# Performance work log

Hardware: AMD Instinct MI355X
Metric: run time of the kernel (lower is better)

The kernel has to match this reference:

```python
import jax, jax.numpy as jnp
import numpy as np

B, S, D = 2, 2048, 1024
H = 16
HD = D // H  # 64


def setup_inputs() -> dict:
    key = jax.random.key(0)
    ks = jax.random.split(key, 9)
    s = 1.0 / np.sqrt(D)
    return {
        "query_input": jax.random.normal(ks[0], (B, S, D), dtype=jnp.float32),
        "Wq": jax.random.normal(ks[1], (D, D), dtype=jnp.float32) * s,
        "bq": jax.random.normal(ks[2], (D,), dtype=jnp.float32) * 0.02,
        "Wk": jax.random.normal(ks[3], (D, D), dtype=jnp.float32) * s,
        "bk": jax.random.normal(ks[4], (D,), dtype=jnp.float32) * 0.02,
        "Wv": jax.random.normal(ks[5], (D, D), dtype=jnp.float32) * s,
        "bv": jax.random.normal(ks[6], (D,), dtype=jnp.float32) * 0.02,
        "Wo": jax.random.normal(ks[7], (D, D), dtype=jnp.float32) * s,
        "bo": jax.random.normal(ks[8], (D,), dtype=jnp.float32) * 0.02,
    }


def _split_heads(x):
    # [B, S, D] -> [B, H, S, HD]
    return x.reshape(B, S, H, HD).transpose(0, 2, 1, 3)


def reference(query_input, Wq, bq, Wk, bk, Wv, bv, Wo, bo):
    # self-attention: key_value_input = query_input
    q = _split_heads(query_input @ Wq + bq)
    k = _split_heads(query_input @ Wk + bk)
    v = _split_heads(query_input @ Wv + bv)
    scores = jnp.einsum("bhqd,bhkd->bhqk", q, k) / jnp.sqrt(jnp.float32(HD))
    probs = jax.nn.softmax(scores, axis=-1)  # dropout is identity in eval
    ctx = jnp.einsum("bhqk,bhkd->bhqd", probs, v)
    ctx = ctx.transpose(0, 2, 1, 3).reshape(B, S, D)
    return ctx @ Wo + bo
```

## Files before the change

### kernel.cpp

```cpp
#include <hip/hip_runtime.h>
#include <hip/hip_bf16.h>
#include <cstdint>

constexpr int Bsz = 2, Seq = 2048, Dim = 1024, NH = 16, HDim = 64;
constexpr int Mtok = Bsz * Seq;
constexpr int NQKV = 3 * Dim;
constexpr float QSCALE = 0.125f * 1.4426950408889634f;

typedef __attribute__((ext_vector_type(4))) float f32x4;
typedef __attribute__((ext_vector_type(16))) float f32x16;
typedef __attribute__((ext_vector_type(8))) short bf16x8;

#if __has_builtin(__builtin_amdgcn_exp2f)
#define EXP2(x) __builtin_amdgcn_exp2f(x)
#else
#define EXP2(x) exp2f(x)
#endif

__device__ __forceinline__ ushort f2bf(float f) {
    union { float f; uint32_t u; } v; v.f = f;
    uint32_t u = v.u;
    uint32_t r = (u + 0x7fffu + ((u >> 16) & 1u)) >> 16;
    return (ushort)r;
}

__device__ __forceinline__ uint cvt_pk_bf16(float lo, float hi) {
    uint r;
    asm("v_cvt_pk_bf16_f32 %0, %1, %2" : "=v"(r) : "v"(lo), "v"(hi));
    return r;
}

__device__ __forceinline__ void gll16(const ushort* g, ushort* l) {
    __builtin_amdgcn_global_load_lds(
        (const __attribute__((address_space(1))) void*)g,
        (__attribute__((address_space(3))) void*)l, 16, 0, 0);
}

__global__ void convert_x(const float* __restrict__ in, ushort* __restrict__ out, int n16) {
    int i = blockIdx.x * 256 + threadIdx.x;
    if (i >= n16) return;
    int e = i * 16;
    int row = e >> 10;
    int k = e & 1023;
    int k0 = k & ~31;
    int c = (k >> 3) & 3;
    int sw = row & 3;
    const float4* p = (const float4*)(in + e);
    float4 a = p[0], b = p[1], c2 = p[2], d = p[3];
    uint4 o0, o1;
    o0.x = (uint)f2bf(a.x) | ((uint)f2bf(a.y) << 16);
    o0.y = (uint)f2bf(a.z) | ((uint)f2bf(a.w) << 16);
    o0.z = (uint)f2bf(b.x) | ((uint)f2bf(b.y) << 16);
    o0.w = (uint)f2bf(b.z) | ((uint)f2bf(b.w) << 16);
    o1.x = (uint)f2bf(c2.x) | ((uint)f2bf(c2.y) << 16);
    o1.y = (uint)f2bf(c2.z) | ((uint)f2bf(c2.w) << 16);
    o1.z = (uint)f2bf(d.x) | ((uint)f2bf(d.y) << 16);
    o1.w = (uint)f2bf(d.z) | ((uint)f2bf(d.w) << 16);
    ushort* dstrow = out + (size_t)row * 1024 + k0;
    *(uint4*)(dstrow + ((c ^ sw) << 3))       = o0;
    *(uint4*)(dstrow + (((c + 1) ^ sw) << 3)) = o1;
}

__global__ void transpose_w4(const float* __restrict__ Wq, const float* __restrict__ Wk,
                             const float* __restrict__ Wv, const float* __restrict__ Wo,
                             ushort* __restrict__ Wtqkv, ushort* __restrict__ Wto) {
    __shared__ float tile[32][33];
    int z = blockIdx.z;
    const float* src = (z == 0) ? Wq : (z == 1) ? Wk : (z == 2) ? Wv : Wo;
    ushort* dst = (z == 3) ? Wto : Wtqkv + (size_t)z * 1024 * 1024;
    float scale = (z == 0) ? QSCALE : 1.f;
    int bx = blockIdx.x * 32, by = blockIdx.y * 32;
    int tx = threadIdx.x, ty = threadIdx.y;
#pragma unroll
    for (int j = 0; j < 32; j += 8)
        tile[ty + j][tx] = src[(size_t)(by + ty + j) * Dim + bx + tx];
    __syncthreads();
    int c = tx >> 3, wn8 = tx & 7;
#pragma unroll
    for (int j = 0; j < 32; j += 8) {
        int n = bx + ty + j;
        dst[(size_t)n * Dim + by + ((c ^ (n & 3)) << 3) + wn8] = f2bf(tile[tx][ty + j] * scale);
    }
}

__global__ void concat_bias(const float* __restrict__ bq, const float* __restrict__ bk,
                            const float* __restrict__ bv, float* __restrict__ dst) {
    int i = blockIdx.x * 256 + threadIdx.x;
    if (i >= NQKV) return;
    float v = (i < 1024) ? bq[i] * QSCALE : (i < 2048 ? bk[i - 1024] : bv[i - 2048]);
    dst[i] = v;
}

template <bool F32OUT>
__global__ __launch_bounds__(256) void gemm_bt(const ushort* __restrict__ A,
                                               const ushort* __restrict__ Bt,
                                               const float* __restrict__ bias,
                                               void* __restrict__ Cout,
                                               int Msz, int Nsz, int Ksz) {
    __shared__ ushort As[2][128 * 32];
    __shared__ ushort Bs[2][128 * 32];
    const int tid = threadIdx.x;
    const int lane = tid & 63, wid = tid >> 6;
    const int wm = wid >> 1, wn = wid & 1;
    const int bm = blockIdx.x * 128, bn = blockIdx.y * 128;
    const int g = lane >> 4, r16 = lane & 15;

    f32x4 acc[4][4] = {};

    const int srow = tid >> 2;
    const int sc = tid & 3;
    const ushort* ga0 = A + (size_t)(bm + srow) * Ksz + sc * 8;
    const ushort* ga1 = A + (size_t)(bm + 64 + srow) * Ksz + sc * 8;
    const ushort* gb0 = Bt + (size_t)(bn + srow) * Ksz + sc * 8;
    const ushort* gb1 = Bt + (size_t)(bn + 64 + srow) * Ksz + sc * 8;
    const int lofs = wid << 9;

#define GSTAGE(bufi, k_)  do {                          \
        gll16(ga0 + (k_), &As[bufi][lofs]);             \
        gll16(ga1 + (k_), &As[bufi][2048 + lofs]);      \
        gll16(gb0 + (k_), &Bs[bufi][lofs]);             \
        gll16(gb1 + (k_), &Bs[bufi][2048 + lofs]);      \
    } while (0)

    GSTAGE(0, 0);
    int cur = 0;

    for (int k0 = 0; k0 < Ksz; k0 += 32) {
        __syncthreads();
        if (k0 + 32 < Ksz) GSTAGE(cur ^ 1, k0 + 32);
        const ushort* Asb = As[cur];
        const ushort* Bsb = Bs[cur];
        bf16x8 af[4], bfr[4];
#pragma unroll
        for (int mt = 0; mt < 4; mt++) {
            int row = wm * 64 + mt * 16 + r16;
            af[mt] = *(const bf16x8*)(Asb + row * 32 + ((g ^ (row & 3)) * 8));
        }
#pragma unroll
        for (int nt = 0; nt < 4; nt++) {
            int row = wn * 64 + nt * 16 + r16;
            bfr[nt] = *(const bf16x8*)(Bsb + row * 32 + ((g ^ (row & 3)) * 8));
        }
#pragma unroll
        for (int mt = 0; mt < 4; mt++)
#pragma unroll
            for (int nt = 0; nt < 4; nt++)
                acc[mt][nt] = __builtin_amdgcn_mfma_f32_16x16x32_bf16(af[mt], bfr[nt], acc[mt][nt], 0, 0, 0);
        cur ^= 1;
    }
#undef GSTAGE

#pragma unroll
    for (int nt = 0; nt < 4; nt++) {
        int col = bn + wn * 64 + nt * 16 + r16;
        float bv = bias[col];
#pragma unroll
        for (int mt = 0; mt < 4; mt++) {
            int row0 = bm + wm * 64 + mt * 16 + g * 4;
            f32x4 c = acc[mt][nt];
#pragma unroll
            for (int i = 0; i < 4; i++) {
                float v = c[i] + bv;
                if (F32OUT)
                    ((float*)Cout)[(size_t)(row0 + i) * Nsz + col] = v;
                else
                    ((ushort*)Cout)[(size_t)(row0 + i) * Nsz + col] = f2bf(v);
            }
        }
    }
}

__global__ __launch_bounds__(256) void pack_kv(const ushort* __restrict__ QKV,
                                               ushort* __restrict__ Kp,
                                               ushort* __restrict__ Vp) {
    __shared__ ushort t[64][72];
    int bh = blockIdx.y, b = bh >> 4, h = bh & 15;
    int s0 = blockIdx.x * 64;
    int tid = threadIdx.x;
    int r = tid >> 2, c = tid & 3;
    const ushort* ksrc = QKV + (size_t)(b * Seq + s0 + r) * NQKV + 1024 + h * 64;
    ushort* kdst = Kp + ((size_t)bh * Seq + s0 + r) * 64;
    int sw = r & 7;
    *(uint4*)(kdst + ((c ^ sw) * 8))       = *(const uint4*)(ksrc + c * 8);
    *(uint4*)(kdst + (((c + 4) ^ sw) * 8)) = *(const uint4*)(ksrc + (c + 4) * 8);
    const ushort* vsrc = QKV + (size_t)(b * Seq + s0 + r) * NQKV + 2048 + h * 64;
    *(uint4*)(&t[r][c * 16])     = *(const uint4*)(vsrc + c * 16);
    *(uint4*)(&t[r][c * 16 + 8]) = *(const uint4*)(vsrc + c * 16 + 8);
    __syncthreads();
    int d = tid >> 2, cq = tid & 3;
    uint u[8];
#pragma unroll
    for (int jj = 0; jj < 8; jj++)
        u[jj] = (uint)t[cq * 16 + jj * 2][d] | ((uint)t[cq * 16 + jj * 2 + 1][d] << 16);
    int swd = d & 7;
    ushort* vdst = Vp + ((size_t)bh * Seq + s0) * 64 + d * 64;
    *(uint4*)(vdst + (((cq * 2) ^ swd) * 8))     = make_uint4(u[0], u[1], u[2], u[3]);
    *(uint4*)(vdst + (((cq * 2 + 1) ^ swd) * 8)) = make_uint4(u[4], u[5], u[6], u[7]);
}

__global__ __launch_bounds__(256) void attn(const ushort* __restrict__ QKV,
                                            const ushort* __restrict__ Kp,
                                            const ushort* __restrict__ Vp,
                                            ushort* __restrict__ Ctx) {
    __shared__ ushort Ks[2][64 * 64];
    __shared__ ushort Vs[2][64 * 64];
    __shared__ float Rl[4][32];
    const int tid = threadIdx.x, lane = tid & 63, w = tid >> 6;
    const int bh = blockIdx.y, b = bh >> 4, h = bh & 15;
    const int l31 = lane & 31, hi = lane >> 5, sw7 = l31 & 7;
    const bool lo = (hi == 0);
    const int qrow = blockIdx.x * 128 + w * 32;

    const ushort* Qr = QKV + (size_t)(b * Seq + qrow + l31) * NQKV + h * 64;
    bf16x8 qf[4];
#pragma unroll
    for (int ks = 0; ks < 4; ks++)
        qf[ks] = *(const bf16x8*)(Qr + ks * 16 + hi * 8);

    const ushort* KpB = Kp + (size_t)bh * Seq * 64;
    const ushort* VpB = Vp + (size_t)bh * Seq * 64;
    const int wb = w * 512;

#define STAGE(bufi, kv0_)  do {                                        \
        const ushort* ks_ = KpB + (size_t)(kv0_) * 64 + tid * 8;       \
        const ushort* vs_ = VpB + (size_t)(kv0_) * 64 + tid * 8;       \
        gll16(ks_,        &Ks[bufi][wb]);                              \
        gll16(ks_ + 2048, &Ks[bufi][2048 + wb]);                       \
        gll16(vs_,        &Vs[bufi][wb]);                              \
        gll16(vs_ + 2048, &Vs[bufi][2048 + wb]);                       \
    } while (0)

    STAGE(0, 0);

    f32x16 c0 = {}, c1 = {};
    float l_run = 0.f;
    int cur = 0;

    for (int kv0 = 0; kv0 < Seq; kv0 += 64) {
        __syncthreads();
        if (kv0 + 64 < Seq) STAGE(cur ^ 1, kv0 + 64);
        const ushort* Kt = Ks[cur];
        const ushort* Vt = Vs[cur];

        f32x16 s0, s1;
#pragma unroll
        for (int r = 0; r < 16; r++) { s0[r] = -8.f; s1[r] = -8.f; }
        __builtin_amdgcn_s_setprio(1);
#pragma unroll
        for (int ks = 0; ks < 4; ks++) {
            int ch = ((ks * 2 + hi) ^ sw7) << 3;
            bf16x8 k0 = *(const bf16x8*)(Kt + l31 * 64 + ch);
            bf16x8 k1 = *(const bf16x8*)(Kt + (32 + l31) * 64 + ch);
            s0 = __builtin_amdgcn_mfma_f32_32x32x16_bf16(k0, qf[ks], s0, 0, 0, 0);
            s1 = __builtin_amdgcn_mfma_f32_32x32x16_bf16(k1, qf[ks], s1, 0, 0, 0);
        }
        __builtin_amdgcn_s_setprio(0);

        float p0[16], p1[16];
        float ls0 = 0.f, ls1 = 0.f;
#pragma unroll
        for (int r = 0; r < 16; r++) {
            p0[r] = EXP2(s0[r]);
            p1[r] = EXP2(s1[r]);
            ls0 += p0[r]; ls1 += p1[r];
        }
        l_run += ls0 + ls1;

        bf16x8 pa[4];
#pragma unroll
        for (int sl = 0; sl < 4; sl++) {
            const float* pp = (sl < 2) ? p0 : p1;
            int rb = (sl & 1) * 8;
            uint x  = cvt_pk_bf16(pp[rb + 0], pp[rb + 1]);
            uint x2 = cvt_pk_bf16(pp[rb + 2], pp[rb + 3]);
            uint y  = cvt_pk_bf16(pp[rb + 4], pp[rb + 5]);
            uint y2 = cvt_pk_bf16(pp[rb + 6], pp[rb + 7]);
            uint v1 = lo ? y : x;
            uint v2 = lo ? y2 : x2;
            uint sv1 = (uint)__shfl_xor((int)v1, 32);
            uint sv2 = (uint)__shfl_xor((int)v2, 32);
            union { uint u[4]; bf16x8 v; } fr;
            fr.u[0] = lo ? x  : sv1;
            fr.u[1] = lo ? x2 : sv2;
            fr.u[2] = lo ? sv1 : y;
            fr.u[3] = lo ? sv2 : y2;
            pa[sl] = fr.v;
        }

        __builtin_amdgcn_s_setprio(1);
#pragma unroll
        for (int sl = 0; sl < 4; sl++) {
            int ch = ((sl * 2 + hi) ^ sw7) << 3;
            bf16x8 vf0 = *(const bf16x8*)(Vt + l31 * 64 + ch);
            bf16x8 vf1 = *(const bf16x8*)(Vt + (32 + l31) * 64 + ch);
            c0 = __builtin_amdgcn_mfma_f32_32x32x16_bf16(pa[sl], vf0, c0, 0, 0, 0);
            c1 = __builtin_amdgcn_mfma_f32_32x32x16_bf16(pa[sl], vf1, c1, 0, 0, 0);
        }
        __builtin_amdgcn_s_setprio(0);
        cur ^= 1;
    }
#undef STAGE

    float lt = l_run + __shfl_xor(l_run, 32);
    if (lo) Rl[w][l31] = 1.f / lt;
    __builtin_amdgcn_s_waitcnt(0);
    float rlv[16];
#pragma unroll
    for (int r = 0; r < 16; r++)
        rlv[r] = Rl[w][(r & 3) + 8 * (r >> 2) + 4 * hi];

    const int rowbase = b * Seq + qrow;
    const int cl = l31 >> 3, c7 = l31 & 7;
#pragma unroll
    for (int r = 0; r < 16; r++) {
        int q = (r & 3) + 8 * (r >> 2) + 4 * hi;
        int row = rowbase + q;
        int col0 = h * 64 + ((cl ^ (row & 3)) << 3) + c7;
        int col1 = h * 64 + 32 + ((cl ^ (row & 3)) << 3) + c7;
        Ctx[(size_t)row * Dim + col0] = f2bf(c0[r] * rlv[r]);
        Ctx[(size_t)row * Dim + col1] = f2bf(c1[r] * rlv[r]);
    }
}

extern "C" void kernel_launch(void* const* d_in, const int* in_sizes, int n_in,
                              void* d_out, int out_size, void* d_ws, size_t ws_size,
                              hipStream_t stream) {
    const float* X  = (const float*)d_in[0];
    const float* Wq = (const float*)d_in[1];
    const float* bq = (const float*)d_in[2];
    const float* Wk = (const float*)d_in[3];
    const float* bk = (const float*)d_in[4];
    const float* Wv = (const float*)d_in[5];
    const float* bv = (const float*)d_in[6];
    const float* Wo = (const float*)d_in[7];
    const float* bo = (const float*)d_in[8];

    char* ws = (char*)d_ws;
    ushort* Xb    = (ushort*)(ws);
    ushort* Wtqkv = (ushort*)(ws + 8388608);
    ushort* Wto   = (ushort*)(ws + 14680064);
    float*  bqkv  = (float*)(ws + 16777216);
    ushort* QKVb  = (ushort*)(ws + 16793600);
    ushort* Vp    = (ushort*)(ws + 41959424);
    ushort* Ctxb  = (ushort*)(ws + 50348032);
    ushort* Kp    = Xb;

    convert_x<<<1024, 256, 0, stream>>>(X, Xb, Mtok * Dim / 16);
    transpose_w4<<<dim3(32, 32, 4), dim3(32, 8), 0, stream>>>(Wq, Wk, Wv, Wo, Wtqkv, Wto);
    concat_bias<<<12, 256, 0, stream>>>(bq, bk, bv, bqkv);

    gemm_bt<false><<<dim3(32, 24), 256, 0, stream>>>(Xb, Wtqkv, bqkv, QKVb, Mtok, NQKV, Dim);
    pack_kv<<<dim3(32, 32), 256, 0, stream>>>(QKVb, Kp, Vp);
    attn<<<dim3(16, 32), 256, 0, stream>>>(QKVb, Kp, Vp, Ctxb);
    gemm_bt<true><<<dim3(32, 8), 256, 0, stream>>>(Ctxb, Wto, bo, (float*)d_out, Mtok, Dim, Dim);
}
```

Measured before the change: 135.9 us.

## Split attention KV range in two and add a combine kernel

Attention is split along the key/value sequence into two halves via blockIdx.z, doubling the block count from 512 to 1024 so the 256 CUs get more work and better occupancy. Each half writes unnormalized fp32 partial context and row sums. A new combine kernel adds the halves, normalizes, and writes the swizzled bf16 context. This works because the kernel uses a fixed max offset rather than a running max. The cost is extra fp32 traffic (about 32 MB written and read) and one more kernel launch.

Result: slower. 146.1 us (+7.5%).

```diff
diff --git a/kernel.cpp b/kernel.cpp
--- a/kernel.cpp
+++ b/kernel.cpp
@@ -201,15 +201,18 @@
 __global__ __launch_bounds__(256) void attn(const ushort* __restrict__ QKV,
                                             const ushort* __restrict__ Kp,
                                             const ushort* __restrict__ Vp,
-                                            ushort* __restrict__ Ctx) {
+                                            float* __restrict__ P0,
+                                            float* __restrict__ P1,
+                                            float* __restrict__ Lb) {
     __shared__ ushort Ks[2][64 * 64];
     __shared__ ushort Vs[2][64 * 64];
-    __shared__ float Rl[4][32];
     const int tid = threadIdx.x, lane = tid & 63, w = tid >> 6;
     const int bh = blockIdx.y, b = bh >> 4, h = bh & 15;
+    const int z = blockIdx.z;
     const int l31 = lane & 31, hi = lane >> 5, sw7 = l31 & 7;
     const bool lo = (hi == 0);
     const int qrow = blockIdx.x * 128 + w * 32;
+    const int kvbeg = z << 10, kvend = kvbeg + 1024;
 
     const ushort* Qr = QKV + (size_t)(b * Seq + qrow + l31) * NQKV + h * 64;
     bf16x8 qf[4];
@@ -230,15 +233,15 @@
         gll16(vs_ + 2048, &Vs[bufi][2048 + wb]);                       \
     } while (0)
 
-    STAGE(0, 0);
+    STAGE(0, kvbeg);
 
     f32x16 c0 = {}, c1 = {};
     float l_run = 0.f;
     int cur = 0;
 
-    for (int kv0 = 0; kv0 < Seq; kv0 += 64) {
+    for (int kv0 = kvbeg; kv0 < kvend; kv0 += 64) {
         __syncthreads();
-        if (kv0 + 64 < Seq) STAGE(cur ^ 1, kv0 + 64);
+        if (kv0 + 64 < kvend) STAGE(cur ^ 1, kv0 + 64);
         const ushort* Kt = Ks[cur];
         const ushort* Vt = Vs[cur];
 
@@ -302,24 +305,37 @@
 #undef STAGE
 
     float lt = l_run + __shfl_xor(l_run, 32);
-    if (lo) Rl[w][l31] = 1.f / lt;
-    __builtin_amdgcn_s_waitcnt(0);
-    float rlv[16];
-#pragma unroll
-    for (int r = 0; r < 16; r++)
-        rlv[r] = Rl[w][(r & 3) + 8 * (r >> 2) + 4 * hi];
-
     const int rowbase = b * Seq + qrow;
-    const int cl = l31 >> 3, c7 = l31 & 7;
+    if (lo) Lb[((size_t)z * Mtok + rowbase + l31) * NH + h] = lt;
+    float* Pout = z ? P1 : P0;
 #pragma unroll
     for (int r = 0; r < 16; r++) {
         int q = (r & 3) + 8 * (r >> 2) + 4 * hi;
-        int row = rowbase + q;
-        int col0 = h * 64 + ((cl ^ (row & 3)) << 3) + c7;
-        int col1 = h * 64 + 32 + ((cl ^ (row & 3)) << 3) + c7;
-        Ctx[(size_t)row * Dim + col0] = f2bf(c0[r] * rlv[r]);
-        Ctx[(size_t)row * Dim + col1] = f2bf(c1[r] * rlv[r]);
-    }
+        size_t row = rowbase + q;
+        Pout[row * Dim + h * 64 + l31]      = c0[r];
+        Pout[row * Dim + h * 64 + 32 + l31] = c1[r];
+    }
+}
+
+__global__ __launch_bounds__(256) void combine(const float* __restrict__ P0,
+                                               const float* __restrict__ P1,
+                                               const float* __restrict__ Lb,
+                                               ushort* __restrict__ Ctx) {
+    int idx = blockIdx.x * 256 + threadIdx.x;
+    int row = idx >> 7, ch = idx & 127;
+    int colb = ch * 8, h = ch >> 3;
+    const float4* a = (const float4*)(P0 + (size_t)row * Dim + colb);
+    const float4* bp = (const float4*)(P1 + (size_t)row * Dim + colb);
+    float l = Lb[(size_t)row * NH + h] + Lb[(size_t)Mtok * NH + (size_t)row * NH + h];
+    float rl = 1.f / l;
+    float4 x0 = a[0], x1 = a[1], y0 = bp[0], y1 = bp[1];
+    uint4 o;
+    o.x = (uint)f2bf((x0.x + y0.x) * rl) | ((uint)f2bf((x0.y + y0.y) * rl) << 16);
+    o.y = (uint)f2bf((x0.z + y0.z) * rl) | ((uint)f2bf((x0.w + y0.w) * rl) << 16);
+    o.z = (uint)f2bf((x1.x + y1.x) * rl) | ((uint)f2bf((x1.y + y1.y) * rl) << 16);
+    o.w = (uint)f2bf((x1.z + y1.z) * rl) | ((uint)f2bf((x1.w + y1.w) * rl) << 16);
+    int cc = (colb >> 3) & 3, base = colb & ~31;
+    *(uint4*)(Ctx + (size_t)row * Dim + base + ((cc ^ (row & 3)) << 3)) = o;
 }
 
 extern "C" void kernel_launch(void* const* d_in, const int* in_sizes, int n_in,
@@ -343,7 +359,10 @@
     ushort* QKVb  = (ushort*)(ws + 16793600);
     ushort* Vp    = (ushort*)(ws + 41959424);
     ushort* Ctxb  = (ushort*)(ws + 50348032);
+    float*  P1    = (float*)(ws + 58736640);
+    float*  Lb    = (float*)(ws + 75513856);
     ushort* Kp    = Xb;
+    float*  P0    = (float*)d_out;
 
     convert_x<<<1024, 256, 0, stream>>>(X, Xb, Mtok * Dim / 16);
     transpose_w4<<<dim3(32, 32, 4), dim3(32, 8), 0, stream>>>(Wq, Wk, Wv, Wo, Wtqkv, Wto);
@@ -351,6 +370,7 @@
 
     gemm_bt<false><<<dim3(32, 24), 256, 0, stream>>>(Xb, Wtqkv, bqkv, QKVb, Mtok, NQKV, Dim);
     pack_kv<<<dim3(32, 32), 256, 0, stream>>>(QKVb, Kp, Vp);
-    attn<<<dim3(16, 32), 256, 0, stream>>>(QKVb, Kp, Vp, Ctxb);
+    attn<<<dim3(16, 32, 2), 256, 0, stream>>>(QKVb, Kp, Vp, P0, P1, Lb);
+    combine<<<Mtok * 128 / 256, 256, 0, stream>>>(P0, P1, Lb, Ctxb);
     gemm_bt<true><<<dim3(32, 8), 256, 0, stream>>>(Ctxb, Wto, bo, (float*)d_out, Mtok, Dim, Dim);
 }
```

## Fuse K/V head packing into QKV GEMM epilogue and use permlane32 swap

Applied to the files above, without the earlier changes.

The QKV projection GEMM now writes Q, K and V directly in the per-head swizzled layouts the attention kernel expects, so the separate pack_kv kernel and its extra read/write pass over K and V go away. Each kernel gets its own buffer in the workspace. Separately, the attention kernel replaces two shfl_xor plus select sequences with v_permlane32_swap when building the P fragments, cutting cross-lane traffic. The trade-off is that the K epilogue now does scattered 2-byte stores and V does 8-byte strided stores, which may coalesce worse than the old row-major stores.

New measurement: 130.6 us. 1.04x faster.

```diff
diff --git a/kernel.cpp b/kernel.cpp
--- a/kernel.cpp
+++ b/kernel.cpp
@@ -91,12 +91,12 @@
     dst[i] = v;
 }
 
-template <bool F32OUT>
-__global__ __launch_bounds__(256) void gemm_bt(const ushort* __restrict__ A,
-                                               const ushort* __restrict__ Bt,
-                                               const float* __restrict__ bias,
-                                               void* __restrict__ Cout,
-                                               int Msz, int Nsz, int Ksz) {
+__global__ __launch_bounds__(256) void gemm_qkv(const ushort* __restrict__ A,
+                                                const ushort* __restrict__ Bt,
+                                                const float* __restrict__ bias,
+                                                ushort* __restrict__ Qp,
+                                                ushort* __restrict__ Kp,
+                                                ushort* __restrict__ Vp) {
     __shared__ ushort As[2][128 * 32];
     __shared__ ushort Bs[2][128 * 32];
     const int tid = threadIdx.x;
@@ -104,6 +104,7 @@
     const int wm = wid >> 1, wn = wid & 1;
     const int bm = blockIdx.x * 128, bn = blockIdx.y * 128;
     const int g = lane >> 4, r16 = lane & 15;
+    const int Ksz = Dim;
 
     f32x4 acc[4][4] = {};
 
@@ -154,51 +155,123 @@
     for (int nt = 0; nt < 4; nt++) {
         int col = bn + wn * 64 + nt * 16 + r16;
         float bv = bias[col];
+        if (col < 1024) {
+#pragma unroll
+            for (int mt = 0; mt < 4; mt++) {
+                int row0 = bm + wm * 64 + mt * 16 + g * 4;
+                f32x4 c = acc[mt][nt];
+#pragma unroll
+                for (int i = 0; i < 4; i++)
+                    Qp[(size_t)(row0 + i) * 1024 + col] = f2bf(c[i] + bv);
+            }
+        } else if (col < 2048) {
+            int h = (col - 1024) >> 6, d = (col - 1024) & 63;
+#pragma unroll
+            for (int mt = 0; mt < 4; mt++) {
+                int row0 = bm + wm * 64 + mt * 16 + g * 4;
+                f32x4 c = acc[mt][nt];
+#pragma unroll
+                for (int i = 0; i < 4; i++) {
+                    int row = row0 + i;
+                    int b = row >> 11, s = row & 2047;
+                    size_t idx = ((size_t)(b * 16 + h) * 2048 + s) * 64
+                               + (((d >> 3) ^ (s & 7)) << 3) + (d & 7);
+                    Kp[idx] = f2bf(c[i] + bv);
+                }
+            }
+        } else {
+            int h = (col - 2048) >> 6, dv = (col - 2048) & 63;
+#pragma unroll
+            for (int mt = 0; mt < 4; mt++) {
+                int row0 = bm + wm * 64 + mt * 16 + g * 4;
+                f32x4 c = acc[mt][nt];
+                int b = row0 >> 11, s = row0 & 2047;
+                int s0 = s & ~63, si = s & 63;
+                uint2 pk;
+                pk.x = cvt_pk_bf16(c[0] + bv, c[1] + bv);
+                pk.y = cvt_pk_bf16(c[2] + bv, c[3] + bv);
+                size_t idx = ((size_t)(b * 16 + h) * 2048 + s0) * 64 + dv * 64
+                           + (((si >> 3) ^ (dv & 7)) << 3) + (si & 7);
+                *(uint2*)(Vp + idx) = pk;
+            }
+        }
+    }
+}
+
+__global__ __launch_bounds__(256) void gemm_bt(const ushort* __restrict__ A,
+                                               const ushort* __restrict__ Bt,
+                                               const float* __restrict__ bias,
+                                               float* __restrict__ Cout,
+                                               int Nsz, int Ksz) {
+    __shared__ ushort As[2][128 * 32];
+    __shared__ ushort Bs[2][128 * 32];
+    const int tid = threadIdx.x;
+    const int lane = tid & 63, wid = tid >> 6;
+    const int wm = wid >> 1, wn = wid & 1;
+    const int bm = blockIdx.x * 128, bn = blockIdx.y * 128;
+    const int g = lane >> 4, r16 = lane & 15;
+
+    f32x4 acc[4][4] = {};
+
+    const int srow = tid >> 2;
+    const int sc = tid & 3;
+    const ushort* ga0 = A + (size_t)(bm + srow) * Ksz + sc * 8;
+    const ushort* ga1 = A + (size_t)(bm + 64 + srow) * Ksz + sc * 8;
+    const ushort* gb0 = Bt + (size_t)(bn + srow) * Ksz + sc * 8;
+    const ushort* gb1 = Bt + (size_t)(bn + 64 + srow) * Ksz + sc * 8;
+    const int lofs = wid << 9;
+
+#define GSTAGE(bufi, k_)  do {                          \
+        gll16(ga0 + (k_), &As[bufi][lofs]);             \
+        gll16(ga1 + (k_), &As[bufi][2048 + lofs]);      \
+        gll16(gb0 + (k_), &Bs[bufi][lofs]);             \
+        gll16(gb1 + (k_), &Bs[bufi][2048 + lofs]);      \
+    } while (0)
+
+    GSTAGE(0, 0);
+    int cur = 0;
+
+    for (int k0 = 0; k0 < Ksz; k0 += 32) {
+        __syncthreads();
+        if (k0 + 32 < Ksz) GSTAGE(cur ^ 1, k0 + 32);
+        const ushort* Asb = As[cur];
+        const ushort* Bsb = Bs[cur];
+        bf16x8 af[4], bfr[4];
+#pragma unroll
+        for (int mt = 0; mt < 4; mt++) {
+            int row = wm * 64 + mt * 16 + r16;
+            af[mt] = *(const bf16x8*)(Asb + row * 32 + ((g ^ (row & 3)) * 8));
+        }
+#pragma unroll
+        for (int nt = 0; nt < 4; nt++) {
+            int row = wn * 64 + nt * 16 + r16;
+            bfr[nt] = *(const bf16x8*)(Bsb + row * 32 + ((g ^ (row & 3)) * 8));
+        }
+#pragma unroll
+        for (int mt = 0; mt < 4; mt++)
+#pragma unroll
+            for (int nt = 0; nt < 4; nt++)
+                acc[mt][nt] = __builtin_amdgcn_mfma_f32_16x16x32_bf16(af[mt], bfr[nt], acc[mt][nt], 0, 0, 0);
+        cur ^= 1;
+    }
+#undef GSTAGE
+
+#pragma unroll
+    for (int nt = 0; nt < 4; nt++) {
+        int col = bn + wn * 64 + nt * 16 + r16;
+        float bv = bias[col];
 #pragma unroll
         for (int mt = 0; mt < 4; mt++) {
             int row0 = bm + wm * 64 + mt * 16 + g * 4;
             f32x4 c = acc[mt][nt];
 #pragma unroll
-            for (int i = 0; i < 4; i++) {
-                float v = c[i] + bv;
-                if (F32OUT)
-                    ((float*)Cout)[(size_t)(row0 + i) * Nsz + col] = v;
-                else
-                    ((ushort*)Cout)[(size_t)(row0 + i) * Nsz + col] = f2bf(v);
-            }
-        }
-    }
-}
-
-__global__ __launch_bounds__(256) void pack_kv(const ushort* __restrict__ QKV,
-                                               ushort* __restrict__ Kp,
-                                               ushort* __restrict__ Vp) {
-    __shared__ ushort t[64][72];
-    int bh = blockIdx.y, b = bh >> 4, h = bh & 15;
-    int s0 = blockIdx.x * 64;
-    int tid = threadIdx.x;
-    int r = tid >> 2, c = tid & 3;
-    const ushort* ksrc = QKV + (size_t)(b * Seq + s0 + r) * NQKV + 1024 + h * 64;
-    ushort* kdst = Kp + ((size_t)bh * Seq + s0 + r) * 64;
-    int sw = r & 7;
-    *(uint4*)(kdst + ((c ^ sw) * 8))       = *(const uint4*)(ksrc + c * 8);
-    *(uint4*)(kdst + (((c + 4) ^ sw) * 8)) = *(const uint4*)(ksrc + (c + 4) * 8);
-    const ushort* vsrc = QKV + (size_t)(b * Seq + s0 + r) * NQKV + 2048 + h * 64;
-    *(uint4*)(&t[r][c * 16])     = *(const uint4*)(vsrc + c * 16);
-    *(uint4*)(&t[r][c * 16 + 8]) = *(const uint4*)(vsrc + c * 16 + 8);
-    __syncthreads();
-    int d = tid >> 2, cq = tid & 3;
-    uint u[8];
-#pragma unroll
-    for (int jj = 0; jj < 8; jj++)
-        u[jj] = (uint)t[cq * 16 + jj * 2][d] | ((uint)t[cq * 16 + jj * 2 + 1][d] << 16);
-    int swd = d & 7;
-    ushort* vdst = Vp + ((size_t)bh * Seq + s0) * 64 + d * 64;
-    *(uint4*)(vdst + (((cq * 2) ^ swd) * 8))     = make_uint4(u[0], u[1], u[2], u[3]);
-    *(uint4*)(vdst + (((cq * 2 + 1) ^ swd) * 8)) = make_uint4(u[4], u[5], u[6], u[7]);
-}
-
-__global__ __launch_bounds__(256) void attn(const ushort* __restrict__ QKV,
+            for (int i = 0; i < 4; i++)
+                Cout[(size_t)(row0 + i) * Nsz + col] = c[i] + bv;
+        }
+    }
+}
+
+__global__ __launch_bounds__(256) void attn(const ushort* __restrict__ Qp,
                                             const ushort* __restrict__ Kp,
                                             const ushort* __restrict__ Vp,
                                             ushort* __restrict__ Ctx) {
@@ -211,7 +284,7 @@
     const bool lo = (hi == 0);
     const int qrow = blockIdx.x * 128 + w * 32;
 
-    const ushort* Qr = QKV + (size_t)(b * Seq + qrow + l31) * NQKV + h * 64;
+    const ushort* Qr = Qp + (size_t)(b * Seq + qrow + l31) * 1024 + h * 64;
     bf16x8 qf[4];
 #pragma unroll
     for (int ks = 0; ks < 4; ks++)
@@ -275,15 +348,13 @@
             uint x2 = cvt_pk_bf16(pp[rb + 2], pp[rb + 3]);
             uint y  = cvt_pk_bf16(pp[rb + 4], pp[rb + 5]);
             uint y2 = cvt_pk_bf16(pp[rb + 6], pp[rb + 7]);
-            uint v1 = lo ? y : x;
-            uint v2 = lo ? y2 : x2;
-            uint sv1 = (uint)__shfl_xor((int)v1, 32);
-            uint sv2 = (uint)__shfl_xor((int)v2, 32);
+            asm("v_permlane32_swap_b32 %0, %1" : "+v"(x),  "+v"(y));
+            asm("v_permlane32_swap_b32 %0, %1" : "+v"(x2), "+v"(y2));
             union { uint u[4]; bf16x8 v; } fr;
-            fr.u[0] = lo ? x  : sv1;
-            fr.u[1] = lo ? x2 : sv2;
-            fr.u[2] = lo ? sv1 : y;
-            fr.u[3] = lo ? sv2 : y2;
+            fr.u[0] = x;
+            fr.u[1] = x2;
+            fr.u[2] = y;
+            fr.u[3] = y2;
             pa[sl] = fr.v;
         }
 
@@ -340,17 +411,16 @@
     ushort* Wtqkv = (ushort*)(ws + 8388608);
     ushort* Wto   = (ushort*)(ws + 14680064);
     float*  bqkv  = (float*)(ws + 16777216);
-    ushort* QKVb  = (ushort*)(ws + 16793600);
-    ushort* Vp    = (ushort*)(ws + 41959424);
-    ushort* Ctxb  = (ushort*)(ws + 50348032);
-    ushort* Kp    = Xb;
+    ushort* Qp    = (ushort*)(ws + 16793600);
+    ushort* Kp    = (ushort*)(ws + 25182208);
+    ushort* Vp    = (ushort*)(ws + 33570816);
+    ushort* Ctxb  = (ushort*)(ws + 41959424);
 
     convert_x<<<1024, 256, 0, stream>>>(X, Xb, Mtok * Dim / 16);
     transpose_w4<<<dim3(32, 32, 4), dim3(32, 8), 0, stream>>>(Wq, Wk, Wv, Wo, Wtqkv, Wto);
     concat_bias<<<12, 256, 0, stream>>>(bq, bk, bv, bqkv);
 
-    gemm_bt<false><<<dim3(32, 24), 256, 0, stream>>>(Xb, Wtqkv, bqkv, QKVb, Mtok, NQKV, Dim);
-    pack_kv<<<dim3(32, 32), 256, 0, stream>>>(QKVb, Kp, Vp);
-    attn<<<dim3(16, 32), 256, 0, stream>>>(QKVb, Kp, Vp, Ctxb);
-    gemm_bt<true><<<dim3(32, 8), 256, 0, stream>>>(Ctxb, Wto, bo, (float*)d_out, Mtok, Dim, Dim);
-}
+    gemm_qkv<<<dim3(32, 24), 256, 0, stream>>>(Xb, Wtqkv, bqkv, Qp, Kp, Vp);
+    attn<<<dim3(16, 32), 256, 0, stream>>>(Qp, Kp, Vp, Ctxb);
+    gemm_bt<<<dim3(32, 8), 256, 0, stream>>>(Ctxb, Wto, bo, (float*)d_out, Dim, Dim);
+}
```
